# Kernel tuning notes

Measured on AMD Instinct MI355X. Metric: run time of the kernel, lower is better.

## Reference

```python
import jax, jax.numpy as jnp
import numpy as np

EPS = 1e-5  # torch InstanceNorm2d default eps


def _attend(x_q, x_kv, Wq, Wk, Wv, Wo):
    # x_q, x_kv: [B, N, C]
    B, N, _ = x_q.shape
    q = x_q @ Wq            # [B, N, CH]
    k = x_kv @ Wk           # [B, N, CH]
    v = x_kv @ Wv           # [B, N, CH]
    CH = q.shape[-1]
    # rearrange 'b n c -> n (b c)' : [N, B*CH]; the torch repeat across batch
    # is redundant (same K/V for every query sample), so we keep one copy.
    kcat = jnp.transpose(k, (1, 0, 2)).reshape(N, B * CH)
    vcat = jnp.transpose(v, (1, 0, 2)).reshape(N, B * CH)
    # scores[b, i, j] = sum_n q[b, n, i] * kcat[n, j]  -> [B, CH, B*CH]
    scores = jnp.einsum('bni,nj->bij', q, kcat)
    # InstanceNorm2d(1): per-sample normalization over the (CH, B*CH) plane
    mu = scores.mean(axis=(1, 2), keepdims=True)
    var = scores.var(axis=(1, 2), keepdims=True)  # biased var, matches torch
    scores = (scores - mu) * jax.lax.rsqrt(var + EPS)
    attn = jax.nn.softmax(scores, axis=-1)        # softmax over j (dim=3)
    # ctx[b, n, i] = sum_j attn[b, i, j] * vcat[n, j]  -> [B, N, CH]
    ctx = jnp.einsum('bij,nj->bni', attn, vcat)
    return ctx @ Wo  # [B, N, C]


def setup_inputs() -> dict:
    key = jax.random.key(0)
    k0, k1, k2, k3, k4 = jax.random.split(key, 5)
    C, H = 64, 8
    CH = C * H
    emb = jax.random.normal(k0, (16, 2048, C), dtype=jnp.float32)
    s = 0.02
    Wq = jax.random.normal(k1, (C, CH), dtype=jnp.float32) * s
    Wk = jax.random.normal(k2, (C, CH), dtype=jnp.float32) * s
    Wv = jax.random.normal(k3, (C, CH), dtype=jnp.float32) * s
    Wo = jax.random.normal(k4, (CH, C), dtype=jnp.float32) * s
    return {"emb": emb, "Wq": Wq, "Wk": Wk, "Wv": Wv, "Wo": Wo}


def reference(emb, Wq, Wk, Wv, Wo):
    emb_l, emb_u = jnp.split(emb, 2, axis=0)
    emb_u_sg = jax.lax.stop_gradient(emb_u)  # emb_u is detached in the torch code
    out_u2l = _attend(emb_u_sg, emb_l, Wq, Wk, Wv, Wo)
    out_l2u = _attend(emb_l, emb_u_sg, Wq, Wk, Wv, Wo)
    return jnp.concatenate([out_l2u, out_u2l], axis=0)
```

## Files before the change

### kernel.cpp

```cpp
#include <hip/hip_runtime.h>
#include <hip/hip_fp16.h>

#define EPS 1e-5f

typedef __attribute__((ext_vector_type(8))) _Float16 half8;
typedef __attribute__((ext_vector_type(4))) float float4v;

__device__ __forceinline__ float rv_from(const float* sums2, int db)
{
    float s1 = 0.f, s2 = 0.f;
#pragma unroll
    for (int p = 0; p < 8; p++) {
        s1 += sums2[(db * 8 + p) * 2];
        s2 += sums2[(db * 8 + p) * 2 + 1];
    }
    const float inv = 1.f / 2097152.f;
    float mu = s1 * inv;
    float var = s2 * inv - mu * mu;
    return rsqrtf(var + EPS);
}

__global__ __launch_bounds__(256)
void prep_k(const float* __restrict__ emb, const float* __restrict__ Wq,
            const float* __restrict__ Wk, const float* __restrict__ Wv,
            const float* __restrict__ Wo, float* __restrict__ Gpart,
            __half* __restrict__ WkT16, __half* __restrict__ Wo16,
            __half* __restrict__ Wv16, float* __restrict__ GWQpart,
            float* __restrict__ wsp, __half* __restrict__ WqT16h,
            __half* __restrict__ WqT16l)
{
    __shared__ __align__(16) char smem[18432];
    const int tid = threadIdx.x;
    const int bid = blockIdx.x;

    if (bid < 512) {
        __half (*As)[72] = (__half(*)[72])smem;
        __half (*Bs)[72] = (__half(*)[72])(smem + 9216);
        const int ks = bid >> 6;
        const int z6 = bid & 63;
        const int b  = z6 >> 3;
        const int bp = z6 & 7;
        const float* Xq  = emb + (long long)b * 131072;
        const float* Xkv = emb + 1048576 + (long long)bp * 131072;

        const int lane = tid & 63, w = tid >> 6, q = lane >> 4, l16 = lane & 15;
        const int tok = tid & 63;
        const int cg  = w * 16;

        float4v acc[4];
#pragma unroll
        for (int nt = 0; nt < 4; nt++) acc[nt] = (float4v)0.f;

        for (int t0 = ks * 256; t0 < ks * 256 + 256; t0 += 64) {
            const float* q4 = Xq  + (long long)(t0 + tok) * 64 + cg;
            const float* k4 = Xkv + (long long)(t0 + tok) * 64 + cg;
#pragma unroll
            for (int j = 0; j < 4; j++) {
                float4 v = *(const float4*)(q4 + j * 4);
                As[cg + j * 4 + 0][tok] = __float2half(v.x);
                As[cg + j * 4 + 1][tok] = __float2half(v.y);
                As[cg + j * 4 + 2][tok] = __float2half(v.z);
                As[cg + j * 4 + 3][tok] = __float2half(v.w);
                float4 u = *(const float4*)(k4 + j * 4);
                Bs[cg + j * 4 + 0][tok] = __float2half(u.x);
                Bs[cg + j * 4 + 1][tok] = __float2half(u.y);
                Bs[cg + j * 4 + 2][tok] = __float2half(u.z);
                Bs[cg + j * 4 + 3][tok] = __float2half(u.w);
            }
            __syncthreads();
#pragma unroll
            for (int kc = 0; kc < 64; kc += 32) {
                half8 af = *(const half8*)&As[w * 16 + l16][kc + q * 8];
                half8 bf[4];
#pragma unroll
                for (int nt = 0; nt < 4; nt++)
                    bf[nt] = *(const half8*)&Bs[nt * 16 + l16][kc + q * 8];
#pragma unroll
                for (int nt = 0; nt < 4; nt++)
                    acc[nt] = __builtin_amdgcn_mfma_f32_16x16x32_f16(af, bf[nt], acc[nt], 0, 0, 0);
            }
            __syncthreads();
        }

        float* Gz = Gpart + (long long)ks * 262144 + (long long)z6 * 4096;
#pragma unroll
        for (int nt = 0; nt < 4; nt++)
#pragma unroll
            for (int t = 0; t < 4; t++) {
                int m = w * 16 + q * 4 + t;
                Gz[m * 64 + nt * 16 + l16] = acc[nt][t];
            }
    } else if (bid < 528) {
        float (*t)[65] = (float(*)[65])smem;
        const int which = (bid - 512) >> 3;
        const int c0 = ((bid - 512) & 7) * 64;
        const int c = tid & 63, r4 = tid >> 6;
        if (which == 0) {
#pragma unroll
            for (int rr = r4; rr < 64; rr += 4)
                t[rr][c] = Wk[rr * 512 + c0 + c];
            __syncthreads();
#pragma unroll
            for (int rr = r4; rr < 64; rr += 4)
                WkT16[(c0 + rr) * 64 + c] = __float2half(t[c][rr]);
        } else {
#pragma unroll
            for (int rr = r4; rr < 64; rr += 4)
                t[rr][c] = Wo[(c0 + rr) * 64 + c];
            __syncthreads();
#pragma unroll
            for (int rr = r4; rr < 64; rr += 4)
                Wo16[rr * 512 + c0 + c] = __float2half(t[c][rr]);
        }
    } else if (bid < 536) {
        const int base = (bid - 528) * 4096;
#pragma unroll
        for (int it = 0; it < 4; it++) {
            int e = base + (tid + it * 256) * 4;
            float4 v = *(const float4*)(Wv + e);
            *(__half2*)(Wv16 + e)     = __floats2half2_rn(v.x, v.y);
            *(__half2*)(Wv16 + e + 2) = __floats2half2_rn(v.z, v.w);
        }
    } else if (bid < 552) {
        float (*Wl)[68] = (float(*)[68])smem;
        const int t2 = bid - 536;
        const int which = t2 >> 3;
        const int sl = t2 & 7;
        const int i0 = sl * 64;
        const float* W = which ? Wq : Wk;
        float* Gout = GWQpart + (long long)(which * 8 + sl) * 4096;
#pragma unroll
        for (int it = 0; it < 4; it++) {
            int e = tid + it * 256;
            int cc = e >> 4, i4 = (e & 15) * 4;
            *(float4*)&Wl[cc][i4] = *(const float4*)(W + cc * 512 + i0 + i4);
        }
        __syncthreads();
        if (tid < 64) {
            float s = 0.f;
#pragma unroll
            for (int j = 0; j < 64; j++) s += Wl[tid][j];
            wsp[(which * 8 + sl) * 64 + tid] = s;
        }
        const int cr = tid >> 2, cg = (tid & 3) * 16;
        float p[16] = {};
        for (int k = 0; k < 64; k++) {
            float a = Wl[cr][k];
#pragma unroll
            for (int j = 0; j < 16; j++) p[j] += a * Wl[cg + j][k];
        }
#pragma unroll
        for (int j = 0; j < 16; j++)
            Gout[cr * 64 + cg + j] = p[j];
    } else {
        float (*t)[65] = (float(*)[65])smem;
        const int i0 = (bid - 552) * 64;
        const int c = tid & 63, r4 = tid >> 6;
#pragma unroll
        for (int rr = r4; rr < 64; rr += 4)
            t[rr][c] = Wq[rr * 512 + i0 + c];
        __syncthreads();
#pragma unroll
        for (int rr = r4; rr < 64; rr += 4) {
            float x = t[c][rr];
            __half h = __float2half(x);
            WqT16h[(i0 + rr) * 64 + c] = h;
            WqT16l[(i0 + rr) * 64 + c] = __float2half(x - __half2float(h));
        }
    }
}

__global__ __launch_bounds__(256)
void stats2_k(const float* __restrict__ Gpart, const float* __restrict__ GWQpart,
              const float* __restrict__ wsp, __half* __restrict__ GT16h,
              __half* __restrict__ GT16l, float* __restrict__ sums2)
{
    __shared__ float Graw[64][68], Gs[64][68], GQs[64][68], GWs[64][68];
    __shared__ float wqsS[64], wksS[64];
    const int tid = threadIdx.x;
    const int z = blockIdx.x;
    const int d = z >> 6, b = (z >> 3) & 7, bp = z & 7;
    const int zm = d ? (bp * 8 + b) : (b * 8 + bp);

    for (int f = tid * 4; f < 4096; f += 1024) {
        float4 g = make_float4(0.f, 0.f, 0.f, 0.f);
        float4 gw = g, gq = g;
#pragma unroll
        for (int s = 0; s < 8; s++) {
            float4 p = *(const float4*)(Gpart + (long long)s * 262144 + (long long)zm * 4096 + f);
            g.x += p.x; g.y += p.y; g.z += p.z; g.w += p.w;
            float4 w1 = *(const float4*)(GWQpart + (long long)s * 4096 + f);
            gw.x += w1.x; gw.y += w1.y; gw.z += w1.z; gw.w += w1.w;
            float4 q1 = *(const float4*)(GWQpart + (long long)(8 + s) * 4096 + f);
            gq.x += q1.x; gq.y += q1.y; gq.z += q1.z; gq.w += q1.w;
        }
        int rr = f >> 6, cc = f & 63;
        *(float4*)&Graw[rr][cc] = g;
        *(float4*)&GWs[rr][cc] = gw;
        *(float4*)&GQs[rr][cc] = gq;
    }
    if (tid < 64) {
        float a = 0.f, bsum = 0.f;
#pragma unroll
        for (int s = 0; s < 8; s++) {
            bsum += wsp[s * 64 + tid];
            a    += wsp[(8 + s) * 64 + tid];
        }
        wqsS[tid] = a; wksS[tid] = bsum;
    }
    __syncthreads();
    for (int e = tid; e < 4096; e += 256) {
        int rr = e >> 6, cc = e & 63;
        Gs[rr][cc] = d ? Graw[cc][rr] : Graw[rr][cc];
    }
    __syncthreads();
    for (int e = tid; e < 4096; e += 256) {
        int cp = e >> 6, c = e & 63;
        float g = Gs[c][cp];
        __half h = __float2half(g);
        GT16h[(long long)z * 4096 + e] = h;
        GT16l[(long long)z * 4096 + e] = __float2half(g - __half2float(h));
    }

    const int r = tid >> 2;
    const int c0 = (tid & 3) * 16;
    float p1[16] = {}, p2[16] = {};
    for (int k = 0; k < 64; k++) {
        float gq = GQs[r][k], g = Gs[r][k];
#pragma unroll
        for (int j = 0; j < 16; j++) {
            p1[j] += gq * Gs[k][c0 + j];
            p2[j] += g  * GWs[k][c0 + j];
        }
    }
    float s2 = 0.f;
#pragma unroll
    for (int j = 0; j < 16; j++) s2 += p1[j] * p2[j];
    float s1 = 0.f;
    const float wq = wqsS[r];
#pragma unroll
    for (int j = 0; j < 16; j++) s1 += wq * Gs[r][c0 + j] * wksS[c0 + j];

    const int lane = tid & 63, w = tid >> 6;
#pragma unroll
    for (int off = 32; off; off >>= 1) {
        s1 += __shfl_down(s1, off, 64);
        s2 += __shfl_down(s2, off, 64);
    }
    __shared__ float r1[4], r2[4];
    if (lane == 0) { r1[w] = s1; r2[w] = s2; }
    __syncthreads();
    if (tid == 0) {
        sums2[z * 2]     = r1[0] + r1[1] + r1[2] + r1[3];
        sums2[z * 2 + 1] = r2[0] + r2[1] + r2[2] + r2[3];
    }
}

__global__ __launch_bounds__(256)
void mfma_ms(const __half* __restrict__ WqT16h, const __half* __restrict__ WqT16l,
             const __half* __restrict__ GT16h, const __half* __restrict__ GT16l,
             const __half* __restrict__ WkT16, const __half* __restrict__ Wv16,
             const float* __restrict__ sums2, float* __restrict__ rsp,
             __half* __restrict__ Mt)
{
    __shared__ __half Es[128][72];
    __shared__ __half Wks[64][72];
    __shared__ __half Wvs[64][72];
    __shared__ __half Pt[128][72];

    const int tid = threadIdx.x;
    const int z = blockIdx.x;
    const int it = blockIdx.y;
    const int db = z >> 3, bp = z & 7;
    const int i0base = it * 128;

    const int lane = tid & 63, w = tid >> 6, q = lane >> 4, l16 = lane & 15;
    const float rv = rv_from(sums2, db);

    {
        const __half* Wh = WqT16h + (long long)i0base * 64;
        const __half* Wl = WqT16l + (long long)i0base * 64;
        const __half* Gh = GT16h + (long long)z * 4096;
        const __half* Gl = GT16l + (long long)z * 4096;
        float4v eacc[2][4];
#pragma unroll
        for (int a = 0; a < 2; a++)
#pragma unroll
            for (int b2 = 0; b2 < 4; b2++) eacc[a][b2] = (float4v)0.f;
#pragma unroll
        for (int kc = 0; kc < 64; kc += 32) {
            half8 ah[2], al[2], bh[4], bl[4];
#pragma unroll
            for (int mt = 0; mt < 2; mt++) {
                const int i = w * 32 + mt * 16 + l16;
                ah[mt] = *(const half8*)(Wh + i * 64 + kc + q * 8);
                al[mt] = *(const half8*)(Wl + i * 64 + kc + q * 8);
            }
#pragma unroll
            for (int nt = 0; nt < 4; nt++) {
                const int cp = nt * 16 + l16;
                bh[nt] = *(const half8*)(Gh + cp * 64 + kc + q * 8);
                bl[nt] = *(const half8*)(Gl + cp * 64 + kc + q * 8);
            }
#pragma unroll
            for (int mt = 0; mt < 2; mt++)
#pragma unroll
                for (int nt = 0; nt < 4; nt++) {
                    eacc[mt][nt] = __builtin_amdgcn_mfma_f32_16x16x32_f16(ah[mt], bh[nt], eacc[mt][nt], 0, 0, 0);
                    eacc[mt][nt] = __builtin_amdgcn_mfma_f32_16x16x32_f16(ah[mt], bl[nt], eacc[mt][nt], 0, 0, 0);
                    eacc[mt][nt] = __builtin_amdgcn_mfma_f32_16x16x32_f16(al[mt], bh[nt], eacc[mt][nt], 0, 0, 0);
                }
        }
#pragma unroll
        for (int mt = 0; mt < 2; mt++)
#pragma unroll
            for (int nt = 0; nt < 4; nt++)
#pragma unroll
                for (int t = 0; t < 4; t++)
                    Es[w * 32 + mt * 16 + q * 4 + t][nt * 16 + l16] =
                        __float2half(eacc[mt][nt][t]);
    }

    float4v macc[2][4];
#pragma unroll
    for (int a = 0; a < 2; a++)
#pragma unroll
        for (int b2 = 0; b2 < 4; b2++) macc[a][b2] = (float4v)0.f;
    float rsacc[2] = {0.f, 0.f};

    const int srow = tid >> 2, sc8 = (tid & 3) * 16;

    for (int ch0 = 0; ch0 < 512; ch0 += 64) {
        __syncthreads();
        *(half8*)&Wks[srow][sc8]     = *(const half8*)(WkT16 + (long long)(ch0 + srow) * 64 + sc8);
        *(half8*)&Wks[srow][sc8 + 8] = *(const half8*)(WkT16 + (long long)(ch0 + srow) * 64 + sc8 + 8);
        *(half8*)&Wvs[srow][sc8]     = *(const half8*)(Wv16 + (long long)srow * 512 + ch0 + sc8);
        *(half8*)&Wvs[srow][sc8 + 8] = *(const half8*)(Wv16 + (long long)srow * 512 + ch0 + sc8 + 8);
        __syncthreads();

        float4v sacc[4][2];
#pragma unroll
        for (int a = 0; a < 4; a++)
#pragma unroll
            for (int b2 = 0; b2 < 2; b2++) sacc[a][b2] = (float4v)0.f;
#pragma unroll
        for (int kc = 0; kc < 64; kc += 32) {
            half8 af[4], bf[2];
#pragma unroll
            for (int mt = 0; mt < 4; mt++)
                af[mt] = *(const half8*)&Wks[mt * 16 + l16][kc + q * 8];
#pragma unroll
            for (int nt = 0; nt < 2; nt++)
                bf[nt] = *(const half8*)&Es[w * 32 + nt * 16 + l16][kc + q * 8];
#pragma unroll
            for (int mt = 0; mt < 4; mt++)
#pragma unroll
                for (int nt = 0; nt < 2; nt++)
                    sacc[mt][nt] = __builtin_amdgcn_mfma_f32_16x16x32_f16(af[mt], bf[nt], sacc[mt][nt], 0, 0, 0);
        }

#pragma unroll
        for (int nt = 0; nt < 2; nt++) {
            const int i = w * 32 + nt * 16 + l16;
#pragma unroll
            for (int mt = 0; mt < 4; mt++) {
                float e0 = __expf(rv * sacc[mt][nt][0]);
                float e1 = __expf(rv * sacc[mt][nt][1]);
                float e2 = __expf(rv * sacc[mt][nt][2]);
                float e3 = __expf(rv * sacc[mt][nt][3]);
                rsacc[nt] += e0 + e1 + e2 + e3;
                const int ch = mt * 16 + q * 4;
                *(__half2*)&Pt[i][ch]     = __floats2half2_rn(e0, e1);
                *(__half2*)&Pt[i][ch + 2] = __floats2half2_rn(e2, e3);
            }
        }
        __syncthreads();

#pragma unroll
        for (int kc = 0; kc < 64; kc += 32) {
            half8 af2[2], bf2[4];
#pragma unroll
            for (int mt2 = 0; mt2 < 2; mt2++)
                af2[mt2] = *(const half8*)&Pt[w * 32 + mt2 * 16 + l16][kc + q * 8];
#pragma unroll
            for (int nt2 = 0; nt2 < 4; nt2++)
                bf2[nt2] = *(const half8*)&Wvs[nt2 * 16 + l16][kc + q * 8];
#pragma unroll
            for (int mt2 = 0; mt2 < 2; mt2++)
#pragma unroll
                for (int nt2 = 0; nt2 < 4; nt2++)
                    macc[mt2][nt2] = __builtin_amdgcn_mfma_f32_16x16x32_f16(af2[mt2], bf2[nt2], macc[mt2][nt2], 0, 0, 0);
        }
    }

#pragma unroll
    for (int nt = 0; nt < 2; nt++) {
        float p = rsacc[nt];
        p += __shfl_xor(p, 16, 64);
        p += __shfl_xor(p, 32, 64);
        if (q == 0)
            rsp[(long long)(db * 512 + i0base + w * 32 + nt * 16 + l16) * 8 + bp] = p;
    }
    __syncthreads();

    __half (*MtS)[144] = (__half(*)[144])&Pt[0][0];
    const float sc = 1.f / 4096.f;
#pragma unroll
    for (int mt2 = 0; mt2 < 2; mt2++)
#pragma unroll
        for (int nt2 = 0; nt2 < 4; nt2++) {
            const int cp = nt2 * 16 + l16;
            const int il = w * 32 + mt2 * 16 + q * 4;
#pragma unroll
            for (int t = 0; t < 4; t++)
                MtS[cp][il + t] = __float2half(macc[mt2][nt2][t] * sc);
        }
    __syncthreads();
    __half* Mz = Mt + (long long)z * 32768;
    {
        const int row = tid >> 2, seg = (tid & 3) * 32;
#pragma unroll
        for (int j = 0; j < 4; j++)
            *(half8*)(Mz + (long long)row * 512 + i0base + seg + j * 8) =
                *(const half8*)&MtS[row][seg + j * 8];
    }
}

__global__ __launch_bounds__(256)
void mfma_n(const __half* __restrict__ Mt, const __half* __restrict__ Wo16,
            const float* __restrict__ rsp, __half* __restrict__ NT)
{
    __shared__ __half Mts[64][72];
    __shared__ __half Wos[64][72];
    __shared__ float invrS[64];
    const int tid = threadIdx.x;
    const int db = blockIdx.x >> 3, bp = blockIdx.x & 7;
    const __half* Mz = Mt + (long long)(db * 8 + bp) * 32768;
    const int lane = tid & 63, w = tid >> 6, q = lane >> 4, l16 = lane & 15;

    float4v acc[4];
#pragma unroll
    for (int mt = 0; mt < 4; mt++) acc[mt] = (float4v)0.f;

    const int srow = tid >> 2, sc8 = (tid & 3) * 16;

    for (int i0 = 0; i0 < 512; i0 += 64) {
        __syncthreads();
        if (tid < 64) {
            const float* rp = rsp + (long long)(db * 512 + i0 + tid) * 8;
            float4 a = *(const float4*)rp;
            float4 b = *(const float4*)(rp + 4);
            invrS[tid] = 4096.0f / (a.x + a.y + a.z + a.w + b.x + b.y + b.z + b.w);
        }
        __syncthreads();
#pragma unroll
        for (int h = 0; h < 2; h++) {
            half8 v = *(const half8*)(Mz + (long long)srow * 512 + i0 + sc8 + h * 8);
            half8 o;
#pragma unroll
            for (int j = 0; j < 8; j++)
                o[j] = (_Float16)((float)v[j] * invrS[sc8 + h * 8 + j]);
            *(half8*)&Mts[srow][sc8 + h * 8] = o;
            *(half8*)&Wos[srow][sc8 + h * 8] =
                *(const half8*)(Wo16 + (long long)srow * 512 + i0 + sc8 + h * 8);
        }
        __syncthreads();
#pragma unroll
        for (int kc = 0; kc < 64; kc += 32) {
            half8 af[4];
#pragma unroll
            for (int mt = 0; mt < 4; mt++)
                af[mt] = *(const half8*)&Mts[mt * 16 + l16][kc + q * 8];
            half8 bf = *(const half8*)&Wos[w * 16 + l16][kc + q * 8];
#pragma unroll
            for (int mt = 0; mt < 4; mt++)
                acc[mt] = __builtin_amdgcn_mfma_f32_16x16x32_f16(af[mt], bf, acc[mt], 0, 0, 0);
        }
    }

    __half* Nz = NT + (long long)db * 32768;
    const int o = w * 16 + l16;
#pragma unroll
    for (int mt = 0; mt < 4; mt++) {
        const int k = bp * 64 + mt * 16 + q * 4;
        *(__half2*)(Nz + (long long)o * 512 + k)     = __floats2half2_rn(acc[mt][0], acc[mt][1]);
        *(__half2*)(Nz + (long long)o * 512 + k + 2) = __floats2half2_rn(acc[mt][2], acc[mt][3]);
    }
}

__global__ __launch_bounds__(256)
void mfma_out(const float* __restrict__ emb, const __half* __restrict__ NT,
              float* __restrict__ out)
{
    __shared__ __half Xs[128][72];
    __shared__ __half Bs[64][72];
    const int tid = threadIdx.x;
    const int db = blockIdx.y;
    const int d = db >> 3;
    const int n0 = blockIdx.x * 128;
    const float* Xb = emb + (long long)(1 - d) * 1048576;
    const __half* Bz = NT + (long long)db * 32768;

    const int lane = tid & 63, w = tid >> 6, q = lane >> 4, l16 = lane & 15;

    float4v acc[2][4];
#pragma unroll
    for (int a = 0; a < 2; a++)
#pragma unroll
        for (int b = 0; b < 4; b++) acc[a][b] = (float4v)0.f;

    for (int bp = 0; bp < 8; bp++) {
        const float* src = Xb + (long long)bp * 131072 + (long long)n0 * 64;
#pragma unroll
        for (int it = 0; it < 8; it++) {
            int e = (tid + it * 256) * 4;
            int row = e >> 6, col = e & 63;
            float4 v = *(const float4*)(src + (long long)row * 64 + col);
            *(__half2*)&Xs[row][col]     = __floats2half2_rn(v.x, v.y);
            *(__half2*)&Xs[row][col + 2] = __floats2half2_rn(v.z, v.w);
        }
        {
            int o = tid >> 2, c8 = (tid & 3) * 16;
            *(half8*)&Bs[o][c8]     = *(const half8*)(Bz + o * 512 + bp * 64 + c8);
            *(half8*)&Bs[o][c8 + 8] = *(const half8*)(Bz + o * 512 + bp * 64 + c8 + 8);
        }
        __syncthreads();
#pragma unroll
        for (int kc = 0; kc < 64; kc += 32) {
            half8 af[2], bf[4];
#pragma unroll
            for (int mt = 0; mt < 2; mt++)
                af[mt] = *(const half8*)&Xs[w * 32 + mt * 16 + l16][kc + q * 8];
#pragma unroll
            for (int ot = 0; ot < 4; ot++)
                bf[ot] = *(const half8*)&Bs[ot * 16 + l16][kc + q * 8];
#pragma unroll
            for (int mt = 0; mt < 2; mt++)
#pragma unroll
                for (int ot = 0; ot < 4; ot++)
                    acc[mt][ot] = __builtin_amdgcn_mfma_f32_16x16x32_f16(af[mt], bf[ot], acc[mt][ot], 0, 0, 0);
        }
        __syncthreads();
    }

    float* Od = out + (long long)db * 131072;
#pragma unroll
    for (int mt = 0; mt < 2; mt++)
#pragma unroll
        for (int ot = 0; ot < 4; ot++)
#pragma unroll
            for (int t = 0; t < 4; t++) {
                int n = n0 + w * 32 + mt * 16 + q * 4 + t;
                Od[(long long)n * 64 + ot * 16 + l16] = acc[mt][ot][t];
            }
}

extern "C" void kernel_launch(void* const* d_in, const int* in_sizes, int n_in,
                              void* d_out, int out_size, void* d_ws, size_t ws_size,
                              hipStream_t stream)
{
    const float* emb = (const float*)d_in[0];
    const float* Wq  = (const float*)d_in[1];
    const float* Wk  = (const float*)d_in[2];
    const float* Wv  = (const float*)d_in[3];
    const float* Wo  = (const float*)d_in[4];
    float* out = (float*)d_out;
    float* ws  = (float*)d_ws;

    float* Gpart   = ws;
    float* GWQpart = ws + 2097152;
    float* wsp     = ws + 2162688;
    float* sums2   = ws + 2163712;
    __half* GT16h  = (__half*)(ws + 2163968);
    __half* GT16l  = (__half*)(ws + 2426112);
    float* rsp     = ws + 2688256;
    __half* WkT16  = (__half*)(ws + 2753792);
    __half* Wv16   = (__half*)(ws + 2770176);
    __half* Wo16   = (__half*)(ws + 2786560);
    __half* WqT16h = (__half*)(ws + 2802944);
    __half* WqT16l = (__half*)(ws + 2819328);
    __half* Mt     = (__half*)(ws + 2835712);
    __half* NT     = (__half*)(ws + 4932864);

    prep_k<<<560, 256, 0, stream>>>(emb, Wq, Wk, Wv, Wo, Gpart, WkT16, Wo16,
                                    Wv16, GWQpart, wsp, WqT16h, WqT16l);

    stats2_k<<<128, 256, 0, stream>>>(Gpart, GWQpart, wsp, GT16h, GT16l, sums2);

    mfma_ms<<<dim3(128, 4), 256, 0, stream>>>(WqT16h, WqT16l, GT16h, GT16l,
                                              WkT16, Wv16, sums2, rsp, Mt);

    mfma_n<<<128, 256, 0, stream>>>(Mt, Wo16, rsp, NT);

    mfma_out<<<dim3(16, 16), 256, 0, stream>>>(emb, NT, out);
}
```

Baseline: 159.1 us.

## Precompute fp16 and transposed emb copies; read MFMA operands directly from global

Adds a conversion pass that writes emb once as fp16 in both row-major and channel-major (transposed) layouts. The Gram kernel is split out and reads the transposed fp16 copy straight into MFMA fragments, and the output GEMM reads fp16 emb and NT directly from global memory with no LDS staging or barriers. The aim is to remove the repeated fp32 loads, conversions and LDS transposes each block did before. The cost is one more kernel launch, extra workspace traffic for the fp16 copies, and global loads that may be less coalesced or reused than the LDS-staged version.

Measured after the change: 158.6 us. Within noise of the previous version (-0.3%).

```diff
diff --git a/kernel.cpp b/kernel.cpp
--- a/kernel.cpp
+++ b/kernel.cpp
@@ -4,6 +4,7 @@
 #define EPS 1e-5f
 
 typedef __attribute__((ext_vector_type(8))) _Float16 half8;
+typedef __attribute__((ext_vector_type(4))) _Float16 half4;
 typedef __attribute__((ext_vector_type(4))) float float4v;
 
 __device__ __forceinline__ float rv_from(const float* sums2, int db)
@@ -21,79 +22,50 @@
 }
 
 __global__ __launch_bounds__(256)
-void prep_k(const float* __restrict__ emb, const float* __restrict__ Wq,
-            const float* __restrict__ Wk, const float* __restrict__ Wv,
-            const float* __restrict__ Wo, float* __restrict__ Gpart,
-            __half* __restrict__ WkT16, __half* __restrict__ Wo16,
-            __half* __restrict__ Wv16, float* __restrict__ GWQpart,
-            float* __restrict__ wsp, __half* __restrict__ WqT16h,
-            __half* __restrict__ WqT16l)
+void convT_k(const float* __restrict__ emb, const float* __restrict__ Wq,
+             const float* __restrict__ Wk, const float* __restrict__ Wv,
+             const float* __restrict__ Wo, __half* __restrict__ emb16,
+             __half* __restrict__ embT16, __half* __restrict__ WkT16,
+             __half* __restrict__ Wo16, __half* __restrict__ Wv16,
+             float* __restrict__ GWQpart, float* __restrict__ wsp,
+             __half* __restrict__ WqT16h, __half* __restrict__ WqT16l)
 {
     __shared__ __align__(16) char smem[18432];
     const int tid = threadIdx.x;
     const int bid = blockIdx.x;
 
-    if (bid < 512) {
-        __half (*As)[72] = (__half(*)[72])smem;
-        __half (*Bs)[72] = (__half(*)[72])(smem + 9216);
-        const int ks = bid >> 6;
-        const int z6 = bid & 63;
-        const int b  = z6 >> 3;
-        const int bp = z6 & 7;
-        const float* Xq  = emb + (long long)b * 131072;
-        const float* Xkv = emb + 1048576 + (long long)bp * 131072;
-
-        const int lane = tid & 63, w = tid >> 6, q = lane >> 4, l16 = lane & 15;
-        const int tok = tid & 63;
-        const int cg  = w * 16;
-
-        float4v acc[4];
-#pragma unroll
-        for (int nt = 0; nt < 4; nt++) acc[nt] = (float4v)0.f;
-
-        for (int t0 = ks * 256; t0 < ks * 256 + 256; t0 += 64) {
-            const float* q4 = Xq  + (long long)(t0 + tok) * 64 + cg;
-            const float* k4 = Xkv + (long long)(t0 + tok) * 64 + cg;
-#pragma unroll
-            for (int j = 0; j < 4; j++) {
-                float4 v = *(const float4*)(q4 + j * 4);
-                As[cg + j * 4 + 0][tok] = __float2half(v.x);
-                As[cg + j * 4 + 1][tok] = __float2half(v.y);
-                As[cg + j * 4 + 2][tok] = __float2half(v.z);
-                As[cg + j * 4 + 3][tok] = __float2half(v.w);
-                float4 u = *(const float4*)(k4 + j * 4);
-                Bs[cg + j * 4 + 0][tok] = __float2half(u.x);
-                Bs[cg + j * 4 + 1][tok] = __float2half(u.y);
-                Bs[cg + j * 4 + 2][tok] = __float2half(u.z);
-                Bs[cg + j * 4 + 3][tok] = __float2half(u.w);
-            }
-            __syncthreads();
-#pragma unroll
-            for (int kc = 0; kc < 64; kc += 32) {
-                half8 af = *(const half8*)&As[w * 16 + l16][kc + q * 8];
-                half8 bf[4];
-#pragma unroll
-                for (int nt = 0; nt < 4; nt++)
-                    bf[nt] = *(const half8*)&Bs[nt * 16 + l16][kc + q * 8];
-#pragma unroll
-                for (int nt = 0; nt < 4; nt++)
-                    acc[nt] = __builtin_amdgcn_mfma_f32_16x16x32_f16(af, bf[nt], acc[nt], 0, 0, 0);
-            }
-            __syncthreads();
-        }
-
-        float* Gz = Gpart + (long long)ks * 262144 + (long long)z6 * 4096;
-#pragma unroll
-        for (int nt = 0; nt < 4; nt++)
-#pragma unroll
-            for (int t = 0; t < 4; t++) {
-                int m = w * 16 + q * 4 + t;
-                Gz[m * 64 + nt * 16 + l16] = acc[nt][t];
-            }
-    } else if (bid < 528) {
+    if (bid < 256) {
+        __half (*T)[136] = (__half(*)[136])smem;
+        const int bb = bid >> 4;
+        const int t0 = (bid & 15) * 128;
+        const float* src = emb + (long long)bb * 131072 + (long long)t0 * 64;
+        __half* d16 = emb16 + (long long)bb * 131072 + (long long)t0 * 64;
+#pragma unroll
+        for (int it = 0; it < 8; it++) {
+            int e = (tid + it * 256) * 4;
+            int t = e >> 6, c = e & 63;
+            float4 v = *(const float4*)(src + t * 64 + c);
+            half4 h;
+            h[0] = (_Float16)v.x; h[1] = (_Float16)v.y;
+            h[2] = (_Float16)v.z; h[3] = (_Float16)v.w;
+            *(half4*)(d16 + t * 64 + c) = h;
+            T[c + 0][t] = (__half)h[0];
+            T[c + 1][t] = (__half)h[1];
+            T[c + 2][t] = (__half)h[2];
+            T[c + 3][t] = (__half)h[3];
+        }
+        __syncthreads();
+        __half* dT = embT16 + (long long)bb * 131072 + t0;
+#pragma unroll
+        for (int it = 0; it < 4; it++) {
+            int e = (tid + it * 256) * 8;
+            int c = e >> 7, tt = e & 127;
+            *(half8*)(dT + (long long)c * 2048 + tt) = *(const half8*)&T[c][tt];
+        }
+    } else if (bid < 272) {
         float (*t)[65] = (float(*)[65])smem;
-        const int which = (bid - 512) >> 3;
-        const int c0 = ((bid - 512) & 7) * 64;
+        const int which = (bid - 256) >> 3;
+        const int c0 = ((bid - 256) & 7) * 64;
         const int c = tid & 63, r4 = tid >> 6;
         if (which == 0) {
 #pragma unroll
@@ -112,8 +84,8 @@
             for (int rr = r4; rr < 64; rr += 4)
                 Wo16[rr * 512 + c0 + c] = __float2half(t[c][rr]);
         }
-    } else if (bid < 536) {
-        const int base = (bid - 528) * 4096;
+    } else if (bid < 280) {
+        const int base = (bid - 272) * 4096;
 #pragma unroll
         for (int it = 0; it < 4; it++) {
             int e = base + (tid + it * 256) * 4;
@@ -121,9 +93,9 @@
             *(__half2*)(Wv16 + e)     = __floats2half2_rn(v.x, v.y);
             *(__half2*)(Wv16 + e + 2) = __floats2half2_rn(v.z, v.w);
         }
-    } else if (bid < 552) {
+    } else if (bid < 296) {
         float (*Wl)[68] = (float(*)[68])smem;
-        const int t2 = bid - 536;
+        const int t2 = bid - 280;
         const int which = t2 >> 3;
         const int sl = t2 & 7;
         const int i0 = sl * 64;
@@ -154,7 +126,7 @@
             Gout[cr * 64 + cg + j] = p[j];
     } else {
         float (*t)[65] = (float(*)[65])smem;
-        const int i0 = (bid - 552) * 64;
+        const int i0 = (bid - 296) * 64;
         const int c = tid & 63, r4 = tid >> 6;
 #pragma unroll
         for (int rr = r4; rr < 64; rr += 4)
@@ -168,6 +140,45 @@
             WqT16l[(i0 + rr) * 64 + c] = __float2half(x - __half2float(h));
         }
     }
+}
+
+__global__ __launch_bounds__(256)
+void gram_k(const __half* __restrict__ embT16, float* __restrict__ Gpart)
+{
+    const int tid = threadIdx.x, bid = blockIdx.x;
+    const int ks = bid >> 6, z6 = bid & 63;
+    const int b = z6 >> 3, bp = z6 & 7;
+    const int lane = tid & 63, w = tid >> 6, q = lane >> 4, l16 = lane & 15;
+
+    const __half* Arow = embT16 + (long long)b * 131072 +
+                         (long long)(w * 16 + l16) * 2048 + ks * 256 + q * 8;
+    const __half* Bbase = embT16 + 1048576 + (long long)bp * 131072 +
+                          (long long)l16 * 2048 + ks * 256 + q * 8;
+
+    float4v acc[4];
+#pragma unroll
+    for (int nt = 0; nt < 4; nt++) acc[nt] = (float4v)0.f;
+
+#pragma unroll
+    for (int t0 = 0; t0 < 256; t0 += 32) {
+        half8 af = *(const half8*)(Arow + t0);
+        half8 bf[4];
+#pragma unroll
+        for (int nt = 0; nt < 4; nt++)
+            bf[nt] = *(const half8*)(Bbase + nt * 32768 + t0);
+#pragma unroll
+        for (int nt = 0; nt < 4; nt++)
+            acc[nt] = __builtin_amdgcn_mfma_f32_16x16x32_f16(af, bf[nt], acc[nt], 0, 0, 0);
+    }
+
+    float* Gz = Gpart + (long long)ks * 262144 + (long long)z6 * 4096;
+#pragma unroll
+    for (int nt = 0; nt < 4; nt++)
+#pragma unroll
+        for (int t = 0; t < 4; t++) {
+            int m = w * 16 + q * 4 + t;
+            Gz[m * 64 + nt * 16 + l16] = acc[nt][t];
+        }
 }
 
 __global__ __launch_bounds__(256)
@@ -489,16 +500,14 @@
 }
 
 __global__ __launch_bounds__(256)
-void mfma_out(const float* __restrict__ emb, const __half* __restrict__ NT,
+void mfma_out(const __half* __restrict__ emb16, const __half* __restrict__ NT,
               float* __restrict__ out)
 {
-    __shared__ __half Xs[128][72];
-    __shared__ __half Bs[64][72];
     const int tid = threadIdx.x;
     const int db = blockIdx.y;
     const int d = db >> 3;
     const int n0 = blockIdx.x * 128;
-    const float* Xb = emb + (long long)(1 - d) * 1048576;
+    const __half* Xb = emb16 + (long long)(1 - d) * 1048576;
     const __half* Bz = NT + (long long)db * 32768;
 
     const int lane = tid & 63, w = tid >> 6, q = lane >> 4, l16 = lane & 15;
@@ -510,37 +519,22 @@
         for (int b = 0; b < 4; b++) acc[a][b] = (float4v)0.f;
 
     for (int bp = 0; bp < 8; bp++) {
-        const float* src = Xb + (long long)bp * 131072 + (long long)n0 * 64;
-#pragma unroll
-        for (int it = 0; it < 8; it++) {
-            int e = (tid + it * 256) * 4;
-            int row = e >> 6, col = e & 63;
-            float4 v = *(const float4*)(src + (long long)row * 64 + col);
-            *(__half2*)&Xs[row][col]     = __floats2half2_rn(v.x, v.y);
-            *(__half2*)&Xs[row][col + 2] = __floats2half2_rn(v.z, v.w);
-        }
-        {
-            int o = tid >> 2, c8 = (tid & 3) * 16;
-            *(half8*)&Bs[o][c8]     = *(const half8*)(Bz + o * 512 + bp * 64 + c8);
-            *(half8*)&Bs[o][c8 + 8] = *(const half8*)(Bz + o * 512 + bp * 64 + c8 + 8);
-        }
-        __syncthreads();
+        const __half* src = Xb + (long long)bp * 131072 + (long long)n0 * 64;
 #pragma unroll
         for (int kc = 0; kc < 64; kc += 32) {
             half8 af[2], bf[4];
 #pragma unroll
             for (int mt = 0; mt < 2; mt++)
-                af[mt] = *(const half8*)&Xs[w * 32 + mt * 16 + l16][kc + q * 8];
+                af[mt] = *(const half8*)(src + (long long)(w * 32 + mt * 16 + l16) * 64 + kc + q * 8);
 #pragma unroll
             for (int ot = 0; ot < 4; ot++)
-                bf[ot] = *(const half8*)&Bs[ot * 16 + l16][kc + q * 8];
+                bf[ot] = *(const half8*)(Bz + (long long)(ot * 16 + l16) * 512 + bp * 64 + kc + q * 8);
 #pragma unroll
             for (int mt = 0; mt < 2; mt++)
 #pragma unroll
                 for (int ot = 0; ot < 4; ot++)
                     acc[mt][ot] = __builtin_amdgcn_mfma_f32_16x16x32_f16(af[mt], bf[ot], acc[mt][ot], 0, 0, 0);
         }
-        __syncthreads();
     }
 
     float* Od = out + (long long)db * 131072;
@@ -581,9 +575,14 @@
     __half* WqT16l = (__half*)(ws + 2819328);
     __half* Mt     = (__half*)(ws + 2835712);
     __half* NT     = (__half*)(ws + 4932864);
-
-    prep_k<<<560, 256, 0, stream>>>(emb, Wq, Wk, Wv, Wo, Gpart, WkT16, Wo16,
-                                    Wv16, GWQpart, wsp, WqT16h, WqT16l);
+    __half* emb16  = (__half*)(ws + 5195008);
+    __half* embT16 = (__half*)(ws + 6243584);
+
+    convT_k<<<304, 256, 0, stream>>>(emb, Wq, Wk, Wv, Wo, emb16, embT16,
+                                     WkT16, Wo16, Wv16, GWQpart, wsp,
+                                     WqT16h, WqT16l);
+
+    gram_k<<<512, 256, 0, stream>>>(embT16, Gpart);
 
     stats2_k<<<128, 256, 0, stream>>>(Gpart, GWQpart, wsp, GT16h, GT16l, sums2);
 
@@ -592,5 +591,5 @@
 
     mfma_n<<<128, 256, 0, stream>>>(Mt, Wo16, rsp, NT);
 
-    mfma_out<<<dim3(16, 16), 256, 0, stream>>>(emb, NT, out);
-}
+    mfma_out<<<dim3(16, 16), 256, 0, stream>>>(emb16, NT, out);
+}
```
